# Optimization experiments

Hardware: AMD Instinct MI355X
Metric: run time of the kernel (lower is better)

The kernel has to match this reference:

```python
import jax, jax.numpy as jnp
import numpy as np

B, S, D, H = 2, 2048, 1024, 16
DEPTH = D // H

def setup_inputs() -> dict:
    key = jax.random.key(0)
    ks = jax.random.split(key, 11)
    def glorot(k, shape):
        lim = np.sqrt(6.0 / (shape[0] + shape[1]))
        return jax.random.uniform(k, shape, jnp.float32, -lim, lim)
    return {
        'q': jax.random.normal(ks[0], (B, S, D), jnp.float32),
        'k': jax.random.normal(ks[1], (B, S, D), jnp.float32),
        'v': jax.random.normal(ks[2], (B, S, D), jnp.float32),
        'wq': glorot(ks[3], (D, D)), 'bq': jnp.zeros((D,), jnp.float32),
        'wk': glorot(ks[4], (D, D)), 'bk': jnp.zeros((D,), jnp.float32),
        'wv': glorot(ks[5], (D, D)), 'bv': jnp.zeros((D,), jnp.float32),
        'wo': glorot(ks[6], (D, D)), 'bo': jnp.zeros((D,), jnp.float32),
    }

def _split_heads(x):
    # [B,S,D] -> [B,H,S,depth]
    return x.reshape(B, S, H, DEPTH).transpose(0, 2, 1, 3)

def reference(q, k, v, wq, bq, wk, bk, wv, bv, wo, bo):
    qh = _split_heads(q @ wq + bq)
    kh = _split_heads(k @ wk + bk)
    vh = _split_heads(v @ wv + bv)
    scale = 1.0 / jnp.sqrt(jnp.float32(DEPTH))
    scores = jnp.einsum('bhqd,bhkd->bhqk', qh, kh) * scale
    attn = jax.nn.softmax(scores, axis=-1)
    out = jnp.einsum('bhqk,bhkd->bhqd', attn, vh)  # [B,H,S,depth]
    out = out.transpose(0, 2, 1, 3).reshape(B, S, D)
    return out @ wo + bo
```

## Files before the change

### kernel.cpp

```cpp
#include <hip/hip_runtime.h>
#include <hip/hip_bf16.h>
#include <stdint.h>

#define Bb 2
#define Ss 2048
#define Dd 1024
#define Hh 16

typedef __hip_bfloat16 bf16;
typedef __attribute__((ext_vector_type(8))) short bf16x8;
typedef __attribute__((ext_vector_type(4))) short short4v;
typedef __attribute__((ext_vector_type(4))) float f32x4;

__device__ __forceinline__ void gl_lds16(const void* g, void* l) {
  __builtin_amdgcn_global_load_lds((const __attribute__((address_space(1))) void*)g,
                                   (__attribute__((address_space(3))) void*)l, 16, 0, 0);
}

__device__ __forceinline__ short bf16_bits(float f) {
  union { bf16 h; short s; } u;
  u.h = __float2bfloat16(f);
  return u.s;
}

__device__ __forceinline__ bf16x8 lds_frag(const char* base, int row, int cl) {
  int phys = cl ^ (row & 7);
  return *(const bf16x8*)(base + row * 128 + phys * 16);
}

__global__ void convert_f32_bf16(const float* __restrict__ src, bf16* __restrict__ dst) {
  int i = blockIdx.x * 256 + threadIdx.x;
  const f32x4* s = (const f32x4*)src;
  f32x4 v0 = s[i * 2], v1 = s[i * 2 + 1];
  bf16x8 o;
#pragma unroll
  for (int j = 0; j < 4; j++) { o[j] = bf16_bits(v0[j]); o[j + 4] = bf16_bits(v1[j]); }
  *(bf16x8*)((char*)dst + (size_t)i * 16) = o;
}

template <bool CF32>
__device__ __forceinline__ void gemm_core(const bf16* __restrict__ A, const bf16* __restrict__ WT,
                                          const float* __restrict__ bias, void* __restrict__ Cv,
                                          char* As, char* Bs) {
  const int K = 1024, N = 1024;
  int tid = threadIdx.x, lane = tid & 63, w = tid >> 6;
  int quad = lane >> 4, l16 = lane & 15;
  int m0 = (blockIdx.x & 31) * 128, n0 = (blockIdx.x >> 5) * 128;
  int wm = (w >> 1) * 64, wn = (w & 1) * 64;
  f32x4 acc[4][4] = {};
  for (int k0 = 0; k0 < K; k0 += 64) {
    __syncthreads();
#pragma unroll
    for (int i = 0; i < 4; i++) {
      int c = i * 256 + tid;
      int row = c >> 3, cc = c & 7;
      int gcol = (cc ^ (row & 7)) * 16;
      gl_lds16((const char*)A + ((size_t)(m0 + row) * K + k0) * 2 + gcol, As + c * 16);
      gl_lds16((const char*)WT + ((size_t)(n0 + row) * K + k0) * 2 + gcol, Bs + c * 16);
    }
    __syncthreads();
#pragma unroll
    for (int ks = 0; ks < 2; ks++) {
      bf16x8 a[4], b[4];
#pragma unroll
      for (int mt = 0; mt < 4; mt++) a[mt] = lds_frag(As, wm + mt * 16 + l16, ks * 4 + quad);
#pragma unroll
      for (int nt = 0; nt < 4; nt++) b[nt] = lds_frag(Bs, wn + nt * 16 + l16, ks * 4 + quad);
#pragma unroll
      for (int mt = 0; mt < 4; mt++)
#pragma unroll
        for (int nt = 0; nt < 4; nt++)
          acc[mt][nt] = __builtin_amdgcn_mfma_f32_16x16x32_bf16(a[mt], b[nt], acc[mt][nt], 0, 0, 0);
    }
  }
#pragma unroll
  for (int nt = 0; nt < 4; nt++) {
    int col = n0 + wn + nt * 16 + l16;
    float bv = bias[col];
#pragma unroll
    for (int mt = 0; mt < 4; mt++) {
      int row = m0 + wm + mt * 16 + quad * 4;
#pragma unroll
      for (int r = 0; r < 4; r++) {
        float val = acc[mt][nt][r] + bv;
        size_t idx = (size_t)(row + r) * N + col;
        if (CF32) ((float*)Cv)[idx] = val;
        else      ((bf16*)Cv)[idx] = __float2bfloat16(val);
      }
    }
  }
}

__global__ __launch_bounds__(256, 2) void gemm_bb(const bf16* A, const bf16* WT,
                                                  const float* bias, bf16* C) {
  __shared__ char As[128 * 128], Bs[128 * 128];
  gemm_core<false>(A, WT, bias, C, As, Bs);
}
__global__ __launch_bounds__(256, 2) void gemm_bf(const bf16* A, const bf16* WT,
                                                  const float* bias, float* C) {
  __shared__ char As[128 * 128], Bs[128 * 128];
  gemm_core<true>(A, WT, bias, C, As, Bs);
}

__global__ void transpose_w4(const float* w0, const float* w1, const float* w2, const float* w3,
                             bf16* t0, bf16* t1, bf16* t2, bf16* t3) {
  const float* W;
  bf16* T;
  switch (blockIdx.z) {
    case 0: W = w0; T = t0; break;
    case 1: W = w1; T = t1; break;
    case 2: W = w2; T = t2; break;
    default: W = w3; T = t3; break;
  }
  __shared__ bf16 tile[64][65];
  int tx = threadIdx.x, ty = threadIdx.y;
  int r0 = blockIdx.y * 64, c0 = blockIdx.x * 64;
#pragma unroll
  for (int j = 0; j < 16; j++) {
    int r = ty + j * 4;
    tile[r][tx] = __float2bfloat16(W[(size_t)(r0 + r) * 1024 + c0 + tx]);
  }
  __syncthreads();
#pragma unroll
  for (int j = 0; j < 16; j++) {
    int r = ty + j * 4;
    T[(size_t)(c0 + r) * 1024 + r0 + tx] = tile[tx][r];
  }
}

__global__ void transpose_vh(const bf16* __restrict__ V, bf16* __restrict__ Vt) {
  int tx = threadIdx.x, ty = threadIdx.y;
  int bh = blockIdx.y, b = bh >> 4, h = bh & 15;
  int s0 = blockIdx.x * 64;
  __shared__ bf16 tile[64][65];
#pragma unroll
  for (int j = 0; j < 16; j++) {
    int r = ty + 4 * j;
    tile[r][tx] = V[((size_t)(b * Ss + s0 + r)) * Dd + h * 64 + tx];
  }
  __syncthreads();
#pragma unroll
  for (int j = 0; j < 16; j++) {
    int r = ty + 4 * j;
    Vt[((size_t)(bh * 64 + r)) * Ss + s0 + tx] = tile[tx][r];
  }
}

__global__ __launch_bounds__(256, 2) void flash_attn(
    const bf16* __restrict__ Q, const bf16* __restrict__ Kp,
    const bf16* __restrict__ Vt, bf16* __restrict__ O) {
  __shared__ char Qs[128 * 128];
  __shared__ char Ks[64 * 128];
  __shared__ char Vs[64 * 128];
  __shared__ char Ps[128 * 128];
  int tid = threadIdx.x, lane = tid & 63, w = tid >> 6;
  int quad = lane >> 4, l16 = lane & 15;
  int bx = blockIdx.x;
  int bh = bx & 31, b = bh >> 4, h = bh & 15;
  int q0 = (bx >> 5) * 128;

#pragma unroll
  for (int i = 0; i < 4; i++) {
    int c = i * 256 + tid;
    int row = c >> 3, cc = c & 7;
    int gcol = (cc ^ (row & 7)) * 16;
    gl_lds16((const char*)Q + ((size_t)(b * Ss + q0 + row) * Dd + h * 64) * 2 + gcol, Qs + c * 16);
  }

  f32x4 o_acc[2][4] = {};
  f32x4 l_acc[2] = {};
  const float c1 = 0.125f * 1.44269504f;
  bf16x8 ones;
#pragma unroll
  for (int j = 0; j < 8; j++) ones[j] = (short)0x3F80;

  for (int kb = 0; kb < Ss / 64; kb++) {
    __syncthreads();
#pragma unroll
    for (int i = 0; i < 2; i++) {
      int c = i * 256 + tid;
      int row = c >> 3, cc = c & 7;
      int gcol = (cc ^ (row & 7)) * 16;
      gl_lds16((const char*)Kp + ((size_t)(b * Ss + kb * 64 + row) * Dd + h * 64) * 2 + gcol,
               Ks + c * 16);
      gl_lds16((const char*)Vt + ((size_t)(bh * 64 + row) * Ss + kb * 64) * 2 + gcol,
               Vs + c * 16);
    }
    __syncthreads();

    f32x4 s[4][2] = {};
#pragma unroll
    for (int ks = 0; ks < 2; ks++) {
      bf16x8 ak[4], bq[2];
#pragma unroll
      for (int kt = 0; kt < 4; kt++) ak[kt] = lds_frag(Ks, kt * 16 + l16, ks * 4 + quad);
#pragma unroll
      for (int qt = 0; qt < 2; qt++) bq[qt] = lds_frag(Qs, w * 32 + qt * 16 + l16, ks * 4 + quad);
#pragma unroll
      for (int kt = 0; kt < 4; kt++)
#pragma unroll
        for (int qt = 0; qt < 2; qt++)
          s[kt][qt] = __builtin_amdgcn_mfma_f32_16x16x32_bf16(ak[kt], bq[qt], s[kt][qt], 0, 0, 0);
    }

#pragma unroll
    for (int kt = 0; kt < 4; kt++)
#pragma unroll
      for (int qt = 0; qt < 2; qt++) {
        short4v pv;
#pragma unroll
        for (int r = 0; r < 4; r++) pv[r] = bf16_bits(exp2f(s[kt][qt][r] * c1));
        int row = w * 32 + qt * 16 + l16;
        int cchunk = kt * 2 + (quad >> 1);
        int addr = row * 128 + ((cchunk ^ (row & 7)) * 16) + (quad & 1) * 8;
        *(short4v*)(Ps + addr) = pv;
      }

    asm volatile("" ::: "memory");

#pragma unroll
    for (int ks = 0; ks < 2; ks++) {
      bf16x8 ap[2], bv[4];
#pragma unroll
      for (int mt = 0; mt < 2; mt++) ap[mt] = lds_frag(Ps, w * 32 + mt * 16 + l16, ks * 4 + quad);
#pragma unroll
      for (int nt = 0; nt < 4; nt++) bv[nt] = lds_frag(Vs, nt * 16 + l16, ks * 4 + quad);
#pragma unroll
      for (int mt = 0; mt < 2; mt++) {
#pragma unroll
        for (int nt = 0; nt < 4; nt++)
          o_acc[mt][nt] = __builtin_amdgcn_mfma_f32_16x16x32_bf16(ap[mt], bv[nt], o_acc[mt][nt], 0, 0, 0);
        l_acc[mt] = __builtin_amdgcn_mfma_f32_16x16x32_bf16(ap[mt], ones, l_acc[mt], 0, 0, 0);
      }
    }
  }

#pragma unroll
  for (int mt = 0; mt < 2; mt++)
#pragma unroll
    for (int r = 0; r < 4; r++) {
      float inv = 1.0f / l_acc[mt][r];
      int row = q0 + w * 32 + mt * 16 + quad * 4 + r;
#pragma unroll
      for (int nt = 0; nt < 4; nt++) {
        int col = h * 64 + nt * 16 + l16;
        O[(size_t)(b * Ss + row) * Dd + col] = __float2bfloat16(o_acc[mt][nt][r] * inv);
      }
    }
}

extern "C" void kernel_launch(void* const* d_in, const int* in_sizes, int n_in,
                              void* d_out, int out_size, void* d_ws, size_t ws_size,
                              hipStream_t stream) {
  const float* q  = (const float*)d_in[0];
  const float* k  = (const float*)d_in[1];
  const float* v  = (const float*)d_in[2];
  const float* wq = (const float*)d_in[3];
  const float* bq = (const float*)d_in[4];
  const float* wk = (const float*)d_in[5];
  const float* bk = (const float*)d_in[6];
  const float* wv = (const float*)d_in[7];
  const float* bv = (const float*)d_in[8];
  const float* wo = (const float*)d_in[9];
  const float* bo = (const float*)d_in[10];
  float* out = (float*)d_out;

  char* ws = (char*)d_ws;
  const size_t MB = (size_t)1024 * 1024;
  bf16* wtq = (bf16*)(ws + 0 * MB);
  bf16* wtk = (bf16*)(ws + 2 * MB);
  bf16* wtv = (bf16*)(ws + 4 * MB);
  bf16* wto = (bf16*)(ws + 6 * MB);
  bf16* Qb  = (bf16*)(ws + 8 * MB);
  bf16* AO  = (bf16*)(ws + 8 * MB);
  bf16* Kp  = (bf16*)(ws + 16 * MB);
  bf16* Vt  = (bf16*)(ws + 24 * MB);
  bf16* Vb  = (bf16*)((char*)d_out + 0 * MB);
  bf16* Kb  = (bf16*)((char*)d_out + 0 * MB);
  bf16* Vp  = (bf16*)((char*)d_out + 8 * MB);
  bf16* Qp  = (bf16*)((char*)d_out + 8 * MB);

  dim3 tb(64, 4);
  transpose_w4<<<dim3(16, 16, 4), tb, 0, stream>>>(wq, wk, wv, wo, wtq, wtk, wtv, wto);
  convert_f32_bf16<<<2048, 256, 0, stream>>>(v, Vb);
  gemm_bb<<<256, 256, 0, stream>>>(Vb, wtv, bv, Vp);
  transpose_vh<<<dim3(32, 32), tb, 0, stream>>>(Vp, Vt);
  convert_f32_bf16<<<2048, 256, 0, stream>>>(q, Qb);
  gemm_bb<<<256, 256, 0, stream>>>(Qb, wtq, bq, Qp);
  convert_f32_bf16<<<2048, 256, 0, stream>>>(k, Kb);
  gemm_bb<<<256, 256, 0, stream>>>(Kb, wtk, bk, Kp);
  flash_attn<<<512, 256, 0, stream>>>(Qp, Kp, Vt, AO);
  gemm_bf<<<256, 256, 0, stream>>>(AO, wto, bo, out);
}
```

Before: 269.3 us.

## Fuse QKV projections with f32 conversion and V transpose, split-K flash attention

Replaces the three per-input convert+GEMM launches and the separate V transpose with one 768-block QKV GEMM. It converts f32 activations to bf16 while staging into LDS, folds the softmax scale into Q, and writes V directly in transposed layout. Flash attention now has wave pairs split the key range over two key blocks per iteration with 64 query rows per wave, then merges partial O and l through LDS. The output GEMM uses 128x64 tiles to launch more blocks. This removes intermediate round trips and launches, at the cost of rounding via manual bit packing, more registers, and scattered strided stores for V.

```diff
diff --git a/kernel.cpp b/kernel.cpp
--- a/kernel.cpp
+++ b/kernel.cpp
@@ -9,97 +9,23 @@
 
 typedef __hip_bfloat16 bf16;
 typedef __attribute__((ext_vector_type(8))) short bf16x8;
-typedef __attribute__((ext_vector_type(4))) short short4v;
 typedef __attribute__((ext_vector_type(4))) float f32x4;
+typedef __attribute__((ext_vector_type(4))) unsigned uint4v;
+typedef __attribute__((ext_vector_type(2))) unsigned uint2v;
 
 __device__ __forceinline__ void gl_lds16(const void* g, void* l) {
   __builtin_amdgcn_global_load_lds((const __attribute__((address_space(1))) void*)g,
                                    (__attribute__((address_space(3))) void*)l, 16, 0, 0);
 }
 
-__device__ __forceinline__ short bf16_bits(float f) {
-  union { bf16 h; short s; } u;
-  u.h = __float2bfloat16(f);
-  return u.s;
+__device__ __forceinline__ unsigned pack2(float a, float b) {
+  unsigned ua = __builtin_bit_cast(unsigned, a), ub = __builtin_bit_cast(unsigned, b);
+  return ((ua + 0x8000u) >> 16) | ((ub + 0x8000u) & 0xffff0000u);
 }
 
 __device__ __forceinline__ bf16x8 lds_frag(const char* base, int row, int cl) {
   int phys = cl ^ (row & 7);
   return *(const bf16x8*)(base + row * 128 + phys * 16);
-}
-
-__global__ void convert_f32_bf16(const float* __restrict__ src, bf16* __restrict__ dst) {
-  int i = blockIdx.x * 256 + threadIdx.x;
-  const f32x4* s = (const f32x4*)src;
-  f32x4 v0 = s[i * 2], v1 = s[i * 2 + 1];
-  bf16x8 o;
-#pragma unroll
-  for (int j = 0; j < 4; j++) { o[j] = bf16_bits(v0[j]); o[j + 4] = bf16_bits(v1[j]); }
-  *(bf16x8*)((char*)dst + (size_t)i * 16) = o;
-}
-
-template <bool CF32>
-__device__ __forceinline__ void gemm_core(const bf16* __restrict__ A, const bf16* __restrict__ WT,
-                                          const float* __restrict__ bias, void* __restrict__ Cv,
-                                          char* As, char* Bs) {
-  const int K = 1024, N = 1024;
-  int tid = threadIdx.x, lane = tid & 63, w = tid >> 6;
-  int quad = lane >> 4, l16 = lane & 15;
-  int m0 = (blockIdx.x & 31) * 128, n0 = (blockIdx.x >> 5) * 128;
-  int wm = (w >> 1) * 64, wn = (w & 1) * 64;
-  f32x4 acc[4][4] = {};
-  for (int k0 = 0; k0 < K; k0 += 64) {
-    __syncthreads();
-#pragma unroll
-    for (int i = 0; i < 4; i++) {
-      int c = i * 256 + tid;
-      int row = c >> 3, cc = c & 7;
-      int gcol = (cc ^ (row & 7)) * 16;
-      gl_lds16((const char*)A + ((size_t)(m0 + row) * K + k0) * 2 + gcol, As + c * 16);
-      gl_lds16((const char*)WT + ((size_t)(n0 + row) * K + k0) * 2 + gcol, Bs + c * 16);
-    }
-    __syncthreads();
-#pragma unroll
-    for (int ks = 0; ks < 2; ks++) {
-      bf16x8 a[4], b[4];
-#pragma unroll
-      for (int mt = 0; mt < 4; mt++) a[mt] = lds_frag(As, wm + mt * 16 + l16, ks * 4 + quad);
-#pragma unroll
-      for (int nt = 0; nt < 4; nt++) b[nt] = lds_frag(Bs, wn + nt * 16 + l16, ks * 4 + quad);
-#pragma unroll
-      for (int mt = 0; mt < 4; mt++)
-#pragma unroll
-        for (int nt = 0; nt < 4; nt++)
-          acc[mt][nt] = __builtin_amdgcn_mfma_f32_16x16x32_bf16(a[mt], b[nt], acc[mt][nt], 0, 0, 0);
-    }
-  }
-#pragma unroll
-  for (int nt = 0; nt < 4; nt++) {
-    int col = n0 + wn + nt * 16 + l16;
-    float bv = bias[col];
-#pragma unroll
-    for (int mt = 0; mt < 4; mt++) {
-      int row = m0 + wm + mt * 16 + quad * 4;
-#pragma unroll
-      for (int r = 0; r < 4; r++) {
-        float val = acc[mt][nt][r] + bv;
-        size_t idx = (size_t)(row + r) * N + col;
-        if (CF32) ((float*)Cv)[idx] = val;
-        else      ((bf16*)Cv)[idx] = __float2bfloat16(val);
-      }
-    }
-  }
-}
-
-__global__ __launch_bounds__(256, 2) void gemm_bb(const bf16* A, const bf16* WT,
-                                                  const float* bias, bf16* C) {
-  __shared__ char As[128 * 128], Bs[128 * 128];
-  gemm_core<false>(A, WT, bias, C, As, Bs);
-}
-__global__ __launch_bounds__(256, 2) void gemm_bf(const bf16* A, const bf16* WT,
-                                                  const float* bias, float* C) {
-  __shared__ char As[128 * 128], Bs[128 * 128];
-  gemm_core<true>(A, WT, bias, C, As, Bs);
 }
 
 __global__ void transpose_w4(const float* w0, const float* w1, const float* w2, const float* w3,
@@ -128,36 +54,95 @@
   }
 }
 
-__global__ void transpose_vh(const bf16* __restrict__ V, bf16* __restrict__ Vt) {
-  int tx = threadIdx.x, ty = threadIdx.y;
-  int bh = blockIdx.y, b = bh >> 4, h = bh & 15;
-  int s0 = blockIdx.x * 64;
-  __shared__ bf16 tile[64][65];
-#pragma unroll
-  for (int j = 0; j < 16; j++) {
-    int r = ty + 4 * j;
-    tile[r][tx] = V[((size_t)(b * Ss + s0 + r)) * Dd + h * 64 + tx];
-  }
-  __syncthreads();
-#pragma unroll
-  for (int j = 0; j < 16; j++) {
-    int r = ty + 4 * j;
-    Vt[((size_t)(bh * 64 + r)) * Ss + s0 + tx] = tile[tx][r];
+#define SCL 0.180336878f
+__global__ __launch_bounds__(256, 3) void gemm_qkv(
+    const float* __restrict__ q, const float* __restrict__ k, const float* __restrict__ v,
+    const bf16* __restrict__ WTall,
+    const float* __restrict__ bq, const float* __restrict__ bk, const float* __restrict__ bv,
+    bf16* __restrict__ Qp, bf16* __restrict__ Kp, bf16* __restrict__ Vt) {
+  __shared__ char As[128 * 128], Bs[128 * 128];
+  const int K = 1024;
+  int tid = threadIdx.x, lane = tid & 63, w = tid >> 6;
+  int quad = lane >> 4, l16 = lane & 15;
+  int nblk = blockIdx.x % 24, mblk = blockIdx.x / 24;
+  int m0 = mblk * 128, n0 = nblk * 128;
+  int sel = nblk >> 3;
+  int nloc0 = (nblk & 7) * 128;
+  const float* A = (sel == 0) ? q : (sel == 1) ? k : v;
+  const float* bias = (sel == 0) ? bq : (sel == 1) ? bk : bv;
+  int wm = (w >> 1) * 64, wn = (w & 1) * 64;
+  f32x4 acc[4][4] = {};
+  for (int k0 = 0; k0 < K; k0 += 64) {
+    __syncthreads();
+#pragma unroll
+    for (int i = 0; i < 4; i++) {
+      int c = i * 256 + tid;
+      int row = c >> 3, cc = c & 7;
+      int g = cc ^ (row & 7);
+      const float* src = A + (size_t)(m0 + row) * K + k0 + g * 8;
+      f32x4 v0 = *(const f32x4*)src;
+      f32x4 v1 = *(const f32x4*)(src + 4);
+      uint4v o = {pack2(v0[0], v0[1]), pack2(v0[2], v0[3]),
+                  pack2(v1[0], v1[1]), pack2(v1[2], v1[3])};
+      *(uint4v*)(As + c * 16) = o;
+      gl_lds16((const char*)WTall + ((size_t)(n0 + row) * K + k0) * 2 + g * 16, Bs + c * 16);
+    }
+    __syncthreads();
+#pragma unroll
+    for (int ks = 0; ks < 2; ks++) {
+      bf16x8 a[4], b[4];
+#pragma unroll
+      for (int mt = 0; mt < 4; mt++) a[mt] = lds_frag(As, wm + mt * 16 + l16, ks * 4 + quad);
+#pragma unroll
+      for (int nt = 0; nt < 4; nt++) b[nt] = lds_frag(Bs, wn + nt * 16 + l16, ks * 4 + quad);
+#pragma unroll
+      for (int mt = 0; mt < 4; mt++)
+#pragma unroll
+        for (int nt = 0; nt < 4; nt++)
+          acc[mt][nt] = __builtin_amdgcn_mfma_f32_16x16x32_bf16(a[mt], b[nt], acc[mt][nt], 0, 0, 0);
+    }
+  }
+#pragma unroll
+  for (int nt = 0; nt < 4; nt++) {
+    int nloc = nloc0 + wn + nt * 16 + l16;
+    float bvv = bias[nloc];
+#pragma unroll
+    for (int mt = 0; mt < 4; mt++) {
+      int row = m0 + wm + mt * 16 + quad * 4;
+      if (sel == 2) {
+        int d = nloc & 63, h = nloc >> 6;
+        int b_ = row >> 11, s = row & 2047;
+        int bh = b_ * 16 + h;
+        float f0 = acc[mt][nt][0] + bvv, f1 = acc[mt][nt][1] + bvv;
+        float f2 = acc[mt][nt][2] + bvv, f3 = acc[mt][nt][3] + bvv;
+        uint2v pv = {pack2(f0, f1), pack2(f2, f3)};
+        *(uint2v*)((char*)Vt + ((size_t)(bh * 64 + d) * Ss + s) * 2) = pv;
+      } else {
+        bf16* C = (sel == 0) ? Qp : Kp;
+        float scale = (sel == 0) ? SCL : 1.0f;
+#pragma unroll
+        for (int r = 0; r < 4; r++)
+          C[(size_t)(row + r) * 1024 + nloc] = __float2bfloat16((acc[mt][nt][r] + bvv) * scale);
+      }
+    }
   }
 }
 
 __global__ __launch_bounds__(256, 2) void flash_attn(
     const bf16* __restrict__ Q, const bf16* __restrict__ Kp,
     const bf16* __restrict__ Vt, bf16* __restrict__ O) {
-  __shared__ char Qs[128 * 128];
-  __shared__ char Ks[64 * 128];
-  __shared__ char Vs[64 * 128];
-  __shared__ char Ps[128 * 128];
+  __shared__ char lds[80 * 1024];
+  char* Qs = lds;
   int tid = threadIdx.x, lane = tid & 63, w = tid >> 6;
   int quad = lane >> 4, l16 = lane & 15;
   int bx = blockIdx.x;
   int bh = bx & 31, b = bh >> 4, h = bh & 15;
   int q0 = (bx >> 5) * 128;
+  int qw = (w & 1) * 64;
+  int pair = w >> 1;
+  char* Ps = lds + 48 * 1024 + pair * 16 * 1024;
+  const char* Ksb = lds + 16 * 1024 + pair * 16 * 1024;
+  const char* Vsb = Ksb + 8 * 1024;
 
 #pragma unroll
   for (int i = 0; i < 4; i++) {
@@ -167,86 +152,163 @@
     gl_lds16((const char*)Q + ((size_t)(b * Ss + q0 + row) * Dd + h * 64) * 2 + gcol, Qs + c * 16);
   }
 
-  f32x4 o_acc[2][4] = {};
-  f32x4 l_acc[2] = {};
-  const float c1 = 0.125f * 1.44269504f;
+  f32x4 o_acc[4][4] = {};
+  f32x4 l_acc[4] = {};
   bf16x8 ones;
 #pragma unroll
   for (int j = 0; j < 8; j++) ones[j] = (short)0x3F80;
 
-  for (int kb = 0; kb < Ss / 64; kb++) {
-    __syncthreads();
+  for (int kb0 = 0; kb0 < Ss / 64; kb0 += 2) {
+    __syncthreads();
+#pragma unroll
+    for (int i = 0; i < 8; i++) {
+      int c = i * 256 + tid;
+      int bsel = i >> 1;
+      int kbb = kb0 + (i >> 2);
+      int c2 = c & 511;
+      int row = c2 >> 3, cc = c2 & 7;
+      int gcol = (cc ^ (row & 7)) * 16;
+      char* dst = lds + 16 * 1024 + bsel * 8 * 1024 + c2 * 16;
+      if ((bsel & 1) == 0)
+        gl_lds16((const char*)Kp + ((size_t)(b * Ss + kbb * 64 + row) * Dd + h * 64) * 2 + gcol, dst);
+      else
+        gl_lds16((const char*)Vt + ((size_t)(bh * 64 + row) * Ss + kbb * 64) * 2 + gcol, dst);
+    }
+    __syncthreads();
+
+    f32x4 s[4][4] = {};
+#pragma unroll
+    for (int ks = 0; ks < 2; ks++) {
+      bf16x8 ak[4], bq[4];
+#pragma unroll
+      for (int kt = 0; kt < 4; kt++) ak[kt] = lds_frag(Ksb, kt * 16 + l16, ks * 4 + quad);
+#pragma unroll
+      for (int qt = 0; qt < 4; qt++) bq[qt] = lds_frag(Qs, qw + qt * 16 + l16, ks * 4 + quad);
+#pragma unroll
+      for (int kt = 0; kt < 4; kt++)
+#pragma unroll
+        for (int qt = 0; qt < 4; qt++)
+          s[kt][qt] = __builtin_amdgcn_mfma_f32_16x16x32_bf16(ak[kt], bq[qt], s[kt][qt], 0, 0, 0);
+    }
+
+#pragma unroll
+    for (int kt = 0; kt < 4; kt++)
+#pragma unroll
+      for (int qt = 0; qt < 4; qt++) {
+        unsigned lo = pack2(exp2f(s[kt][qt][0]), exp2f(s[kt][qt][1]));
+        unsigned hi = pack2(exp2f(s[kt][qt][2]), exp2f(s[kt][qt][3]));
+        int row = qw + qt * 16 + l16;
+        int cchunk = kt * 2 + (quad >> 1);
+        int addr = row * 128 + ((cchunk ^ (row & 7)) * 16) + (quad & 1) * 8;
+        uint2v pv = {lo, hi};
+        *(uint2v*)(Ps + addr) = pv;
+      }
+
+    asm volatile("" ::: "memory");
+
+#pragma unroll
+    for (int ks = 0; ks < 2; ks++) {
+      bf16x8 ap[4], bv[4];
+#pragma unroll
+      for (int mt = 0; mt < 4; mt++) ap[mt] = lds_frag(Ps, qw + mt * 16 + l16, ks * 4 + quad);
+#pragma unroll
+      for (int nt = 0; nt < 4; nt++) bv[nt] = lds_frag(Vsb, nt * 16 + l16, ks * 4 + quad);
+#pragma unroll
+      for (int mt = 0; mt < 4; mt++) {
+#pragma unroll
+        for (int nt = 0; nt < 4; nt++)
+          o_acc[mt][nt] = __builtin_amdgcn_mfma_f32_16x16x32_bf16(ap[mt], bv[nt], o_acc[mt][nt], 0, 0, 0);
+        l_acc[mt] = __builtin_amdgcn_mfma_f32_16x16x32_bf16(ap[mt], ones, l_acc[mt], 0, 0, 0);
+      }
+    }
+  }
+
+  __syncthreads();
+  float* Obuf = (float*)(lds + 48 * 1024);
+  float* Lbuf = (float*)(lds + 16 * 1024);
+  if (pair == 1) {
+#pragma unroll
+    for (int mt = 0; mt < 4; mt++)
+#pragma unroll
+      for (int r = 0; r < 4; r++) {
+        int qrow = qw + mt * 16 + quad * 4 + r;
+#pragma unroll
+        for (int nt = 0; nt < 4; nt++) Obuf[qrow * 64 + nt * 16 + l16] = o_acc[mt][nt][r];
+        Lbuf[qrow] = l_acc[mt][r];
+      }
+  }
+  __syncthreads();
+  if (pair == 0) {
+#pragma unroll
+    for (int mt = 0; mt < 4; mt++)
+#pragma unroll
+      for (int r = 0; r < 4; r++) {
+        int qrow = qw + mt * 16 + quad * 4 + r;
+        float lt = l_acc[mt][r] + Lbuf[qrow];
+        float inv = 1.0f / lt;
+        int grow = b * Ss + q0 + qrow;
+#pragma unroll
+        for (int nt = 0; nt < 4; nt++) {
+          float val = (o_acc[mt][nt][r] + Obuf[qrow * 64 + nt * 16 + l16]) * inv;
+          O[(size_t)grow * Dd + h * 64 + nt * 16 + l16] = __float2bfloat16(val);
+        }
+      }
+  }
+}
+
+__global__ __launch_bounds__(256, 2) void gemm_out(
+    const bf16* __restrict__ AO, const bf16* __restrict__ WT,
+    const float* __restrict__ bo, float* __restrict__ out) {
+  __shared__ char As[128 * 128], Bs[64 * 128];
+  const int K = 1024;
+  int tid = threadIdx.x, lane = tid & 63, w = tid >> 6;
+  int quad = lane >> 4, l16 = lane & 15;
+  int m0 = (blockIdx.x >> 4) * 128, n0 = (blockIdx.x & 15) * 64;
+  int wm = w * 32;
+  f32x4 acc[2][4] = {};
+  for (int k0 = 0; k0 < K; k0 += 64) {
+    __syncthreads();
+#pragma unroll
+    for (int i = 0; i < 4; i++) {
+      int c = i * 256 + tid;
+      int row = c >> 3, cc = c & 7;
+      int g = (cc ^ (row & 7)) * 16;
+      gl_lds16((const char*)AO + ((size_t)(m0 + row) * K + k0) * 2 + g, As + c * 16);
+    }
 #pragma unroll
     for (int i = 0; i < 2; i++) {
       int c = i * 256 + tid;
       int row = c >> 3, cc = c & 7;
-      int gcol = (cc ^ (row & 7)) * 16;
-      gl_lds16((const char*)Kp + ((size_t)(b * Ss + kb * 64 + row) * Dd + h * 64) * 2 + gcol,
-               Ks + c * 16);
-      gl_lds16((const char*)Vt + ((size_t)(bh * 64 + row) * Ss + kb * 64) * 2 + gcol,
-               Vs + c * 16);
-    }
-    __syncthreads();
-
-    f32x4 s[4][2] = {};
+      int g = (cc ^ (row & 7)) * 16;
+      gl_lds16((const char*)WT + ((size_t)(n0 + row) * K + k0) * 2 + g, Bs + c * 16);
+    }
+    __syncthreads();
 #pragma unroll
     for (int ks = 0; ks < 2; ks++) {
-      bf16x8 ak[4], bq[2];
-#pragma unroll
-      for (int kt = 0; kt < 4; kt++) ak[kt] = lds_frag(Ks, kt * 16 + l16, ks * 4 + quad);
-#pragma unroll
-      for (int qt = 0; qt < 2; qt++) bq[qt] = lds_frag(Qs, w * 32 + qt * 16 + l16, ks * 4 + quad);
-#pragma unroll
-      for (int kt = 0; kt < 4; kt++)
-#pragma unroll
-        for (int qt = 0; qt < 2; qt++)
-          s[kt][qt] = __builtin_amdgcn_mfma_f32_16x16x32_bf16(ak[kt], bq[qt], s[kt][qt], 0, 0, 0);
-    }
-
-#pragma unroll
-    for (int kt = 0; kt < 4; kt++)
-#pragma unroll
-      for (int qt = 0; qt < 2; qt++) {
-        short4v pv;
-#pragma unroll
-        for (int r = 0; r < 4; r++) pv[r] = bf16_bits(exp2f(s[kt][qt][r] * c1));
-        int row = w * 32 + qt * 16 + l16;
-        int cchunk = kt * 2 + (quad >> 1);
-        int addr = row * 128 + ((cchunk ^ (row & 7)) * 16) + (quad & 1) * 8;
-        *(short4v*)(Ps + addr) = pv;
-      }
-
-    asm volatile("" ::: "memory");
-
-#pragma unroll
-    for (int ks = 0; ks < 2; ks++) {
-      bf16x8 ap[2], bv[4];
-#pragma unroll
-      for (int mt = 0; mt < 2; mt++) ap[mt] = lds_frag(Ps, w * 32 + mt * 16 + l16, ks * 4 + quad);
-#pragma unroll
-      for (int nt = 0; nt < 4; nt++) bv[nt] = lds_frag(Vs, nt * 16 + l16, ks * 4 + quad);
-#pragma unroll
-      for (int mt = 0; mt < 2; mt++) {
+      bf16x8 a[2], b[4];
+#pragma unroll
+      for (int mt = 0; mt < 2; mt++) a[mt] = lds_frag(As, wm + mt * 16 + l16, ks * 4 + quad);
+#pragma unroll
+      for (int nt = 0; nt < 4; nt++) b[nt] = lds_frag(Bs, nt * 16 + l16, ks * 4 + quad);
+#pragma unroll
+      for (int mt = 0; mt < 2; mt++)
 #pragma unroll
         for (int nt = 0; nt < 4; nt++)
-          o_acc[mt][nt] = __builtin_amdgcn_mfma_f32_16x16x32_bf16(ap[mt], bv[nt], o_acc[mt][nt], 0, 0, 0);
-        l_acc[mt] = __builtin_amdgcn_mfma_f32_16x16x32_bf16(ap[mt], ones, l_acc[mt], 0, 0, 0);
-      }
-    }
-  }
-
-#pragma unroll
-  for (int mt = 0; mt < 2; mt++)
-#pragma unroll
-    for (int r = 0; r < 4; r++) {
-      float inv = 1.0f / l_acc[mt][r];
-      int row = q0 + w * 32 + mt * 16 + quad * 4 + r;
-#pragma unroll
-      for (int nt = 0; nt < 4; nt++) {
-        int col = h * 64 + nt * 16 + l16;
-        O[(size_t)(b * Ss + row) * Dd + col] = __float2bfloat16(o_acc[mt][nt][r] * inv);
-      }
-    }
+          acc[mt][nt] = __builtin_amdgcn_mfma_f32_16x16x32_bf16(a[mt], b[nt], acc[mt][nt], 0, 0, 0);
+    }
+  }
+#pragma unroll
+  for (int nt = 0; nt < 4; nt++) {
+    int col = n0 + nt * 16 + l16;
+    float bvv = bo[col];
+#pragma unroll
+    for (int mt = 0; mt < 2; mt++) {
+      int row = m0 + wm + mt * 16 + quad * 4;
+#pragma unroll
+      for (int r = 0; r < 4; r++)
+        out[(size_t)(row + r) * 1024 + col] = acc[mt][nt][r] + bvv;
+    }
+  }
 }
 
 extern "C" void kernel_launch(void* const* d_in, const int* in_sizes, int n_in,
@@ -267,28 +329,19 @@
 
   char* ws = (char*)d_ws;
   const size_t MB = (size_t)1024 * 1024;
-  bf16* wtq = (bf16*)(ws + 0 * MB);
+  bf16* wtall = (bf16*)(ws + 0 * MB);
+  bf16* wtq = wtall;
   bf16* wtk = (bf16*)(ws + 2 * MB);
   bf16* wtv = (bf16*)(ws + 4 * MB);
   bf16* wto = (bf16*)(ws + 6 * MB);
-  bf16* Qb  = (bf16*)(ws + 8 * MB);
-  bf16* AO  = (bf16*)(ws + 8 * MB);
+  bf16* Qp  = (bf16*)(ws + 8 * MB);
+  bf16* AO  = Qp;
   bf16* Kp  = (bf16*)(ws + 16 * MB);
   bf16* Vt  = (bf16*)(ws + 24 * MB);
-  bf16* Vb  = (bf16*)((char*)d_out + 0 * MB);
-  bf16* Kb  = (bf16*)((char*)d_out + 0 * MB);
-  bf16* Vp  = (bf16*)((char*)d_out + 8 * MB);
-  bf16* Qp  = (bf16*)((char*)d_out + 8 * MB);
 
   dim3 tb(64, 4);
   transpose_w4<<<dim3(16, 16, 4), tb, 0, stream>>>(wq, wk, wv, wo, wtq, wtk, wtv, wto);
-  convert_f32_bf16<<<2048, 256, 0, stream>>>(v, Vb);
-  gemm_bb<<<256, 256, 0, stream>>>(Vb, wtv, bv, Vp);
-  transpose_vh<<<dim3(32, 32), tb, 0, stream>>>(Vp, Vt);
-  convert_f32_bf16<<<2048, 256, 0, stream>>>(q, Qb);
-  gemm_bb<<<256, 256, 0, stream>>>(Qb, wtq, bq, Qp);
-  convert_f32_bf16<<<2048, 256, 0, stream>>>(k, Kb);
-  gemm_bb<<<256, 256, 0, stream>>>(Kb, wtk, bk, Kp);
+  gemm_qkv<<<768, 256, 0, stream>>>(q, k, v, wtall, bq, bk, bv, Qp, Kp, Vt);
   flash_attn<<<512, 256, 0, stream>>>(Qp, Kp, Vt, AO);
-  gemm_bf<<<256, 256, 0, stream>>>(AO, wto, bo, out);
-}
+  gemm_out<<<512, 256, 0, stream>>>(AO, wto, bo, out);
+}
```

Result: no change. 266.3 us (-1.1%).
